# Kernel tuning notes

Hardware: AMD Instinct MI355X
Metric: run time of the kernel (lower is better)

## Reference

```python
import jax, jax.numpy as jnp
import numpy as np

SR = 44100
PRE_EMPH = 0.97
FRAME_LEN = int(0.02 * SR)      # 882
FRAME_HOP = FRAME_LEN // 2      # 441
N_FFT = 2048
EPS = 1e-10


def setup_inputs() -> dict:
    key = jax.random.key(0)
    k1, k2 = jax.random.split(key)
    waveform = jax.random.normal(k1, (16, 441000), dtype=jnp.float32)
    # librosa mel filterbank is a fixed nonnegative (n_mels, n_fft//2+1) matrix;
    # a random surrogate keeps the math (dense matmul) identical.
    mel_filters = jax.random.uniform(k2, (60, N_FFT // 2 + 1), dtype=jnp.float32)
    return {"waveform": waveform, "mel_filters": mel_filters}


def _mfdwc(waveform, mel_filters):
    dt = waveform.dtype
    # pre-emphasis: y[0]=x[0], y[t]=x[t]-0.97*x[t-1]
    emph = jnp.concatenate(
        [waveform[:, :1], waveform[:, 1:] - PRE_EMPH * waveform[:, :-1]], axis=1)
    L = emph.shape[1]
    n_frames = 1 + (L - FRAME_LEN) // FRAME_HOP  # static
    idx = jnp.arange(n_frames)[:, None] * FRAME_HOP + jnp.arange(FRAME_LEN)[None, :]
    frames = emph[:, idx]                                   # (B, T, 882)
    window = jnp.asarray(np.hamming(FRAME_LEN), dtype=dt)   # (882,)
    windowed = frames * window
    spec = jnp.fft.rfft(windowed, n=N_FFT, axis=-1)         # (B, T, 1025) complex
    power = jnp.real(spec) ** 2 + jnp.imag(spec) ** 2       # |FFT|^2
    mel = jnp.einsum('mf,btf->btm', mel_filters, power)     # (B, T, 60)
    logmel = jnp.log(mel + EPS)
    # 1-level Haar DWT along mel axis (pywt convention, even length):
    # cA = (x_even + x_odd)/sqrt(2), cD = (x_even - x_odd)/sqrt(2)
    sq2 = jnp.sqrt(jnp.asarray(2.0, dt))
    x_even, x_odd = logmel[..., 0::2], logmel[..., 1::2]
    cA = (x_even + x_odd) / sq2                             # (B, T, 30)
    cD = (x_even - x_odd) / sq2                             # (B, T, 30)
    # delta (window=3, edge-padded): d[t] = a[clamp(t+1)] - a[clamp(t-1)]
    fwd = jnp.concatenate([cA[:, 1:], cA[:, -1:]], axis=1)
    bwd = jnp.concatenate([cA[:, :1], cA[:, :-1]], axis=1)
    delta = fwd - bwd
    feats = jnp.concatenate([cA, delta, cD], axis=-1)       # (B, T, 90)
    mean = jnp.mean(feats, axis=1)
    std = jnp.std(feats, axis=1, ddof=1)                    # torch.std unbiased
    return jnp.concatenate([mean, std], axis=1)             # (B, 180)


def reference(waveform, mel_filters):
    return _mfdwc(waveform, mel_filters)
```

## Files before the change

### kernel.cpp

```cpp
#include <hip/hip_runtime.h>
#include <hip/hip_bf16.h>
#include <math.h>

#define FRAME_LEN 882
#define FRAME_HOP 441
#define NFFT 2048
#define NFRAMES 999
#define NBATCH 16
#define NMEL 60
#define WAVE_LEN 441000
#define PRE_EMPH 0.97f
#define EPS 1e-10f
#define NROWS (NBATCH * NFRAMES)
#define NPANEL 999
#define KPAD 1056
#define NKC 33
#define PANEL_ELEMS (NKC * 512)
#define PANEL_BYTES (PANEL_ELEMS * 2)
#define PI_F 3.14159265358979323846f

#define PADI(i) ((i) + ((i) >> 4))

__device__ __forceinline__ int frag_off(int m, int k) {
  return ((k >> 5) * 512) | (((k >> 3) & 3) * 128) | (m * 8) | (k & 7);
}

typedef float vf2 __attribute__((ext_vector_type(2)));
__device__ __forceinline__ vf2 mkv(float x, float y){ vf2 r; r.x = x; r.y = y; return r; }
__device__ __forceinline__ vf2 cmul(vf2 a, vf2 b){ return a.xx * b + mkv(-a.y, a.y) * b.yx; }
__device__ __forceinline__ vf2 rotni(vf2 z){ return mkv(z.y, -z.x); }

__device__ __forceinline__ void dif_group16(vf2* x, vf2 t1, bool zerohi) {
  const vf2 C81 = mkv(0.9238795325f, -0.3826834324f);
  const vf2 C82 = mkv(0.7071067812f, -0.7071067812f);
  const vf2 C83 = mkv(0.3826834324f, -0.9238795325f);
  vf2 w0 = t1, w1 = cmul(t1, C81), w2 = cmul(t1, C82), w3 = cmul(t1, C83);
  vf2 ws1[8] = {w0, w1, w2, w3, rotni(w0), rotni(w1), rotni(w2), rotni(w3)};
  if (zerohi) {
#pragma unroll
    for (int k = 0; k < 8; ++k) x[k + 8] = cmul(x[k], ws1[k]);
  } else {
#pragma unroll
    for (int k = 0; k < 8; ++k) {
      vf2 u = x[k], v = x[k + 8];
      x[k] = u + v;
      x[k + 8] = cmul(u - v, ws1[k]);
    }
  }
  vf2 t2 = cmul(t1, t1);
  vf2 v1 = cmul(t2, C82);
  vf2 ws2[4] = {t2, v1, rotni(t2), rotni(v1)};
#pragma unroll
  for (int h = 0; h < 2; ++h) {
#pragma unroll
    for (int k = 0; k < 4; ++k) {
      vf2 u = x[h*8 + k], v = x[h*8 + k + 4];
      x[h*8 + k] = u + v;
      x[h*8 + k + 4] = cmul(u - v, ws2[k]);
    }
  }
  vf2 t4 = cmul(t2, t2);
  vf2 t4r = rotni(t4);
#pragma unroll
  for (int h = 0; h < 4; ++h) {
    vf2 a = x[h*4 + 0], b = x[h*4 + 2];
    x[h*4 + 0] = a + b; x[h*4 + 2] = cmul(a - b, t4);
    a = x[h*4 + 1]; b = x[h*4 + 3];
    x[h*4 + 1] = a + b; x[h*4 + 3] = cmul(a - b, t4r);
  }
  vf2 t8 = cmul(t4, t4);
#pragma unroll
  for (int j = 0; j < 8; ++j) {
    vf2 a = x[2*j], b = x[2*j + 1];
    x[2*j] = a + b; x[2*j + 1] = cmul(a - b, t8);
  }
}

__device__ __forceinline__ void dif8(vf2* y) {
  const vf2 c1 = mkv(0.7071067812f, -0.7071067812f);
  const vf2 c3 = mkv(-0.7071067812f, -0.7071067812f);
  vf2 u, v;
  u=y[0]; v=y[4]; y[0]=u+v; y[4]=u-v;
  u=y[1]; v=y[5]; y[1]=u+v; y[5]=cmul(u-v, c1);
  u=y[2]; v=y[6]; y[2]=u+v; y[6]=rotni(u-v);
  u=y[3]; v=y[7]; y[3]=u+v; y[7]=cmul(u-v, c3);
  u=y[0]; v=y[2]; y[0]=u+v; y[2]=u-v;
  u=y[1]; v=y[3]; y[1]=u+v; y[3]=rotni(u-v);
  u=y[4]; v=y[6]; y[4]=u+v; y[6]=u-v;
  u=y[5]; v=y[7]; y[5]=u+v; y[7]=rotni(u-v);
  u=y[0]; v=y[1]; y[0]=u+v; y[1]=u-v;
  u=y[2]; v=y[3]; y[2]=u+v; y[3]=u-v;
  u=y[4]; v=y[5]; y[4]=u+v; y[5]=u-v;
  u=y[6]; v=y[7]; y[6]=u+v; y[7]=u-v;
}

__global__ __launch_bounds__(256) void fft_pow_kernel(
    const float* __restrict__ wav, const float* __restrict__ filt,
    __hip_bfloat16* __restrict__ powrF, __hip_bfloat16* __restrict__ filtbF)
{
  __shared__ vf2 lds2[2][NFFT + (NFFT >> 4)];
  const int id = blockIdx.x;

  if (id >= 4000) {
    const int mm = id - 4000;
    __hip_bfloat16* qp = filtbF + (size_t)(mm >> 4) * PANEL_ELEMS;
    const int m = mm & 15;
    for (int k = threadIdx.x; k < KPAD; k += 256) {
      float v = (mm < NMEL && k < 1025) ? filt[mm * 1025 + k] : 0.f;
      qp[frag_off(m, k)] = __float2bfloat16(v);
    }
    return;
  }

  const int t   = threadIdx.x;
  const int fid = t >> 7;
  const int tt  = t & 127;
  vf2* lds = lds2[fid];

  const int P  = id * 2 + fid;
  const int b  = P & 15;
  const int t0 = 2 * (P >> 4), t1f = t0 + 1;
  const bool has1 = (t1f < NFRAMES);
  const float* w = wav + (size_t)b * WAVE_LEN;
  const int s0 = t0 * FRAME_HOP;
  int s1 = t1f * FRAME_HOP;
  if (s1 > WAVE_LEN - FRAME_LEN) s1 = WAVE_LEN - FRAME_LEN;

  vf2 x[16];
  {
    float sB, cB, sD, cD;
    __sincosf(6.283185307179586f * (float)tt / 881.0f, &sB, &cB);
    __sincosf(6.283185307179586f * 128.0f / 881.0f, &sD, &cD);
    vf2 cur  = mkv(cB, sB);
    vf2 step = mkv(cD, sD);
#pragma unroll
    for (int k = 0; k < 7; ++k) {
      int i = k * 128 + tt;
      float v1 = 0.f, v2 = 0.f;
      if (i < FRAME_LEN) {
        float win = 0.54f - 0.46f * cur.x;
        int s = s0 + i;
        float e1 = (s > 0) ? (w[s] - PRE_EMPH * w[s - 1]) : w[s];
        v1 = e1 * win;
        int ss = s1 + i;
        v2 = (w[ss] - PRE_EMPH * w[ss - 1]) * win;
      }
      x[k] = mkv(v1, v2);
      cur = cmul(cur, step);
    }
#pragma unroll
    for (int k = 7; k < 16; ++k) x[k] = mkv(0.f, 0.f);
  }

  {
    float sA, cA;
    __sincosf(-PI_F * (float)tt / 1024.0f, &sA, &cA);
    dif_group16(x, mkv(cA, sA), true);
  }
#pragma unroll
  for (int k = 0; k < 16; ++k) lds[PADI(k * 128 + tt)] = x[k];
  __syncthreads();

  {
    const int Q = tt >> 3, r = tt & 7;
    const int base = Q * 128 + r;
#pragma unroll
    for (int k = 0; k < 16; ++k) x[k] = lds[PADI(base + k * 8)];
    float sA, cA;
    __sincosf(-PI_F * (float)r / 64.0f, &sA, &cA);
    dif_group16(x, mkv(cA, sA), false);
#pragma unroll
    for (int k = 0; k < 16; ++k) lds[PADI(base + k * 8)] = x[k];
  }
  __syncthreads();

  {
    vf2 ya[8], yb[8];
#pragma unroll
    for (int j = 0; j < 8; ++j) {
      ya[j] = lds[PADI(16 * tt + j)];
      yb[j] = lds[PADI(16 * tt + 8 + j)];
    }
    dif8(ya);
    dif8(yb);
    __syncthreads();
    const int r7 = (int)(__brev((unsigned)tt) >> 25);
    const int RA[8] = {0, 8, 4, 12, 2, 10, 6, 14};
    const int RB[8] = {1, 9, 5, 13, 3, 11, 7, 15};
#pragma unroll
    for (int j = 0; j < 8; ++j) {
      lds[PADI(RA[j] * 128 + r7)] = ya[j];
      lds[PADI(RB[j] * 128 + r7)] = yb[j];
    }
  }
  __syncthreads();

  const int r0g = b * NFRAMES + t0;
  const int r1g = r0g + 1;
  __hip_bfloat16* q0 = powrF + (size_t)(r0g >> 4) * PANEL_ELEMS;
  const int m0 = r0g & 15;
  __hip_bfloat16* q1 = powrF + (size_t)(r1g >> 4) * PANEL_ELEMS;
  const int m1 = r1g & 15;
#pragma unroll
  for (int c = 0; c < 8; ++c) {
    int f = c * 128 + tt;
    int mir = (NFFT - f) & (NFFT - 1);
    vf2 z = lds[PADI(f)];
    vf2 y = lds[PADI(mir)];
    float f1r = z.x + y.x, f1i = z.y - y.y;
    float f2r = z.y + y.y, f2i = y.x - z.x;
    float pw1 = 0.25f * (f1r * f1r + f1i * f1i);
    float pw2 = 0.25f * (f2r * f2r + f2i * f2i);
    q0[frag_off(m0, f)] = __float2bfloat16(pw1);
    if (has1) q1[frag_off(m1, f)] = __float2bfloat16(pw2);
  }
  if (tt == 0) {
    vf2 z = lds[PADI(1024)];
    q0[frag_off(m0, 1024)] = __float2bfloat16(z.x * z.x);
    if (has1) q1[frag_off(m1, 1024)] = __float2bfloat16(z.y * z.y);
  }
  if (tt < KPAD - 1025) {
    int f = 1025 + tt;
    q0[frag_off(m0, f)] = __float2bfloat16(0.f);
    if (has1) q1[frag_off(m1, f)] = __float2bfloat16(0.f);
  }
}

typedef __attribute__((ext_vector_type(8))) short short8x;
typedef __attribute__((ext_vector_type(4))) float float4x;

#define PPB 2

__global__ __launch_bounds__(256) void melgemm_kernel(
    const __hip_bfloat16* __restrict__ powrF,
    const __hip_bfloat16* __restrict__ filtbF,
    float* __restrict__ logmelT)
{
  __shared__ __hip_bfloat16 As[2][PANEL_ELEMS];
  const int tid  = threadIdx.x;
  const int wave = tid >> 6, lane = tid & 63;
  const int p0 = blockIdx.x * PPB;

  short8x Breg[NKC];
  {
    const __hip_bfloat16* pB = filtbF + (size_t)wave * PANEL_ELEMS + lane * 8;
#pragma unroll
    for (int kc = 0; kc < NKC; ++kc)
      Breg[kc] = *(const short8x*)(pB + kc * 512);
  }

  auto stage = [&](int buf, int p) {
    const unsigned char* src =
        (const unsigned char*)(powrF + (size_t)p * PANEL_ELEMS);
    unsigned char* dst = (unsigned char*)As[buf];
#pragma unroll
    for (int r = 0; r < 9; ++r) {
      const int off = r * 4096 + tid * 16;
      if (off < PANEL_BYTES) {
        __builtin_amdgcn_global_load_lds(
            (const __attribute__((address_space(1))) unsigned int*)(src + off),
            (__attribute__((address_space(3))) unsigned int*)(dst + off),
            16, 0, 0);
      }
    }
  };

  stage(0, p0);
  __syncthreads();

  const int mel  = wave * 16 + (lane & 15);
  const int rsub = (lane >> 4) * 4;

  for (int i = 0; i < PPB; ++i) {
    const int p = p0 + i;
    if (p >= NPANEL) break;
    const bool more = (i + 1 < PPB) && (p + 1 < NPANEL);
    if (more) stage((i + 1) & 1, p + 1);

    const __hip_bfloat16* A = As[i & 1];
    float4x acc0 = {0.f, 0.f, 0.f, 0.f};
    float4x acc1 = {0.f, 0.f, 0.f, 0.f};
#pragma unroll
    for (int kc = 0; kc < 16; ++kc) {
      short8x a0 = *(const short8x*)(&A[kc * 512 + lane * 8]);
      short8x a1 = *(const short8x*)(&A[(kc + 16) * 512 + lane * 8]);
      acc0 = __builtin_amdgcn_mfma_f32_16x16x32_bf16(a0, Breg[kc], acc0, 0, 0, 0);
      acc1 = __builtin_amdgcn_mfma_f32_16x16x32_bf16(a1, Breg[kc + 16], acc1, 0, 0, 0);
    }
    {
      short8x a = *(const short8x*)(&A[32 * 512 + lane * 8]);
      acc0 = __builtin_amdgcn_mfma_f32_16x16x32_bf16(a, Breg[32], acc0, 0, 0, 0);
    }

    if (mel < NMEL) {
#pragma unroll
      for (int reg = 0; reg < 4; ++reg) {
        int row = p * 16 + rsub + reg;
        float vv = acc0[reg] + acc1[reg];
        logmelT[(size_t)mel * NROWS + row] = __logf(vv + EPS);
      }
    }
    if (more) __syncthreads();
  }
}

__global__ __launch_bounds__(256) void stats_kernel(
    const float* __restrict__ lmT, float* __restrict__ out)
{
  __shared__ float red[4];
  const int j   = blockIdx.x;
  const int b   = blockIdx.y;
  const int tid = threadIdx.x;
  const int base = b * NFRAMES;
  const float inv_sq2 = 0.7071067811865475f;
  const bool v3 = (tid < NFRAMES - 768);

  float f0, f1, f2, f3;
  if (j < 30) {
    const float* e = lmT + (size_t)(2 * j) * NROWS + base;
    const float* o = lmT + (size_t)(2 * j + 1) * NROWS + base;
    f0 = (e[tid]       + o[tid])       * inv_sq2;
    f1 = (e[tid + 256] + o[tid + 256]) * inv_sq2;
    f2 = (e[tid + 512] + o[tid + 512]) * inv_sq2;
    f3 = v3 ? (e[tid + 768] + o[tid + 768]) * inv_sq2 : 0.f;
  } else if (j < 60) {
    const int m = j - 30;
    const float* e = lmT + (size_t)(2 * m) * NROWS + base;
    const float* o = lmT + (size_t)(2 * m + 1) * NROWS + base;
    auto dl = [&](int t) -> float {
      int tp = (t + 1 > NFRAMES - 1) ? (NFRAMES - 1) : (t + 1);
      int tm = (t - 1 < 0) ? 0 : (t - 1);
      return ((e[tp] + o[tp]) - (e[tm] + o[tm])) * inv_sq2;
    };
    f0 = dl(tid);
    f1 = dl(tid + 256);
    f2 = dl(tid + 512);
    f3 = v3 ? dl(tid + 768) : 0.f;
  } else {
    const int m = j - 60;
    const float* e = lmT + (size_t)(2 * m) * NROWS + base;
    const float* o = lmT + (size_t)(2 * m + 1) * NROWS + base;
    f0 = (e[tid]       - o[tid])       * inv_sq2;
    f1 = (e[tid + 256] - o[tid + 256]) * inv_sq2;
    f2 = (e[tid + 512] - o[tid + 512]) * inv_sq2;
    f3 = v3 ? (e[tid + 768] - o[tid + 768]) * inv_sq2 : 0.f;
  }

  float s = f0 + f1 + f2 + f3;
  for (int o2 = 32; o2 > 0; o2 >>= 1) s += __shfl_xor(s, o2, 64);
  if ((tid & 63) == 0) red[tid >> 6] = s;
  __syncthreads();
  float mean = (red[0] + red[1] + red[2] + red[3]) / (float)NFRAMES;
  __syncthreads();

  float d0 = f0 - mean, d1 = f1 - mean, d2 = f2 - mean;
  float d3 = v3 ? (f3 - mean) : 0.f;
  float s2 = d0 * d0 + d1 * d1 + d2 * d2 + d3 * d3;
  for (int o2 = 32; o2 > 0; o2 >>= 1) s2 += __shfl_xor(s2, o2, 64);
  if ((tid & 63) == 0) red[tid >> 6] = s2;
  __syncthreads();
  float var = (red[0] + red[1] + red[2] + red[3]) / (float)(NFRAMES - 1);

  if (tid == 0) {
    out[b * 180 + j]      = mean;
    out[b * 180 + 90 + j] = sqrtf(var);
  }
}

extern "C" void kernel_launch(void* const* d_in, const int* in_sizes, int n_in,
                              void* d_out, int out_size, void* d_ws, size_t ws_size,
                              hipStream_t stream) {
  const float* wav  = (const float*)d_in[0];
  const float* filt = (const float*)d_in[1];
  float* out = (float*)d_out;

  unsigned char* ws = (unsigned char*)d_ws;
  __hip_bfloat16* powrF  = (__hip_bfloat16*)(ws);
  size_t off = (size_t)NPANEL * PANEL_ELEMS * 2;
  __hip_bfloat16* filtbF = (__hip_bfloat16*)(ws + off);
  off += (size_t)4 * PANEL_ELEMS * 2;
  float* logmelT = (float*)(ws + off);

  fft_pow_kernel<<<4064, 256, 0, stream>>>(wav, filt, powrF, filtbF);
  melgemm_kernel<<<500, 256, 0, stream>>>(powrF, filtbF, logmelT);
  stats_kernel<<<dim3(90, NBATCH), 256, 0, stream>>>(logmelT, out);
}
```

Measured before the change: 112.9 us.

## Run each FFT pair on a single 64-thread wavefront with two columns per thread

The FFT kernel moves from 256-thread blocks that each handle two frame pairs with 128 threads apiece to 64-thread blocks that handle one frame pair, with each thread processing two columns (tt and tt+64) at every stage. Having one wavefront per FFT means its three __syncthreads barriers only synchronise a single wave, which lowers barrier cost, and more instruction-level parallelism is available per thread. The cost is roughly double the register pressure per thread, since x and y arrays of 16 complex values are both live, and the grid grows to 8064 small blocks, which may limit occupancy.

```diff
diff --git a/kernel.cpp b/kernel.cpp
--- a/kernel.cpp
+++ b/kernel.cpp
@@ -94,30 +94,28 @@
   u=y[6]; v=y[7]; y[6]=u+v; y[7]=u-v;
 }
 
-__global__ __launch_bounds__(256) void fft_pow_kernel(
+__global__ __launch_bounds__(64, 2) void fft_pow_kernel(
     const float* __restrict__ wav, const float* __restrict__ filt,
     __hip_bfloat16* __restrict__ powrF, __hip_bfloat16* __restrict__ filtbF)
 {
-  __shared__ vf2 lds2[2][NFFT + (NFFT >> 4)];
+  __shared__ vf2 lds[NFFT + (NFFT >> 4)];
   const int id = blockIdx.x;
 
-  if (id >= 4000) {
-    const int mm = id - 4000;
+  if (id >= 8000) {
+    const int mm = id - 8000;
     __hip_bfloat16* qp = filtbF + (size_t)(mm >> 4) * PANEL_ELEMS;
     const int m = mm & 15;
-    for (int k = threadIdx.x; k < KPAD; k += 256) {
+    for (int k = threadIdx.x; k < KPAD; k += 64) {
       float v = (mm < NMEL && k < 1025) ? filt[mm * 1025 + k] : 0.f;
       qp[frag_off(m, k)] = __float2bfloat16(v);
     }
     return;
   }
 
-  const int t   = threadIdx.x;
-  const int fid = t >> 7;
-  const int tt  = t & 127;
-  vf2* lds = lds2[fid];
-
-  const int P  = id * 2 + fid;
+  const int tt = threadIdx.x;
+  const int ub = tt + 64;
+
+  const int P  = id;
   const int b  = P & 15;
   const int t0 = 2 * (P >> 4), t1f = t0 + 1;
   const bool has1 = (t1f < NFRAMES);
@@ -126,71 +124,100 @@
   int s1 = t1f * FRAME_HOP;
   if (s1 > WAVE_LEN - FRAME_LEN) s1 = WAVE_LEN - FRAME_LEN;
 
-  vf2 x[16];
+  vf2 x[16], y[16];
   {
-    float sB, cB, sD, cD;
-    __sincosf(6.283185307179586f * (float)tt / 881.0f, &sB, &cB);
+    float sA, cA, sB, cB, sD, cD;
+    __sincosf(6.283185307179586f * (float)tt / 881.0f, &sA, &cA);
+    __sincosf(6.283185307179586f * (float)ub / 881.0f, &sB, &cB);
     __sincosf(6.283185307179586f * 128.0f / 881.0f, &sD, &cD);
-    vf2 cur  = mkv(cB, sB);
+    vf2 curA = mkv(cA, sA), curB = mkv(cB, sB);
     vf2 step = mkv(cD, sD);
 #pragma unroll
     for (int k = 0; k < 7; ++k) {
-      int i = k * 128 + tt;
-      float v1 = 0.f, v2 = 0.f;
-      if (i < FRAME_LEN) {
-        float win = 0.54f - 0.46f * cur.x;
+      {
+        int i = k * 128 + tt;
+        float win = 0.54f - 0.46f * curA.x;
         int s = s0 + i;
         float e1 = (s > 0) ? (w[s] - PRE_EMPH * w[s - 1]) : w[s];
-        v1 = e1 * win;
+        float v1 = e1 * win;
         int ss = s1 + i;
-        v2 = (w[ss] - PRE_EMPH * w[ss - 1]) * win;
+        float v2 = (w[ss] - PRE_EMPH * w[ss - 1]) * win;
+        x[k] = mkv(v1, v2);
+        curA = cmul(curA, step);
       }
-      x[k] = mkv(v1, v2);
-      cur = cmul(cur, step);
-    }
-#pragma unroll
-    for (int k = 7; k < 16; ++k) x[k] = mkv(0.f, 0.f);
+      {
+        int i = k * 128 + ub;
+        float v1 = 0.f, v2 = 0.f;
+        if (i < FRAME_LEN) {
+          float win = 0.54f - 0.46f * curB.x;
+          int s = s0 + i;
+          v1 = (w[s] - PRE_EMPH * w[s - 1]) * win;
+          int ss = s1 + i;
+          v2 = (w[ss] - PRE_EMPH * w[ss - 1]) * win;
+        }
+        y[k] = mkv(v1, v2);
+        curB = cmul(curB, step);
+      }
+    }
+#pragma unroll
+    for (int k = 7; k < 16; ++k) { x[k] = mkv(0.f, 0.f); y[k] = mkv(0.f, 0.f); }
   }
 
   {
-    float sA, cA;
-    __sincosf(-PI_F * (float)tt / 1024.0f, &sA, &cA);
-    dif_group16(x, mkv(cA, sA), true);
-  }
-#pragma unroll
-  for (int k = 0; k < 16; ++k) lds[PADI(k * 128 + tt)] = x[k];
+    float s_, c_;
+    __sincosf(-PI_F * (float)tt / 1024.0f, &s_, &c_);
+    dif_group16(x, mkv(c_, s_), true);
+    __sincosf(-PI_F * (float)ub / 1024.0f, &s_, &c_);
+    dif_group16(y, mkv(c_, s_), true);
+  }
+#pragma unroll
+  for (int k = 0; k < 16; ++k) {
+    lds[PADI(k * 128 + tt)] = x[k];
+    lds[PADI(k * 128 + ub)] = y[k];
+  }
   __syncthreads();
 
   {
     const int Q = tt >> 3, r = tt & 7;
-    const int base = Q * 128 + r;
-#pragma unroll
-    for (int k = 0; k < 16; ++k) x[k] = lds[PADI(base + k * 8)];
-    float sA, cA;
-    __sincosf(-PI_F * (float)r / 64.0f, &sA, &cA);
-    dif_group16(x, mkv(cA, sA), false);
-#pragma unroll
-    for (int k = 0; k < 16; ++k) lds[PADI(base + k * 8)] = x[k];
+    const int baseA = Q * 128 + r;
+    const int baseB = baseA + 1024;
+#pragma unroll
+    for (int k = 0; k < 16; ++k) x[k] = lds[PADI(baseA + k * 8)];
+#pragma unroll
+    for (int k = 0; k < 16; ++k) y[k] = lds[PADI(baseB + k * 8)];
+    float s_, c_;
+    __sincosf(-PI_F * (float)r / 64.0f, &s_, &c_);
+    vf2 t1 = mkv(c_, s_);
+    dif_group16(x, t1, false);
+    dif_group16(y, t1, false);
+#pragma unroll
+    for (int k = 0; k < 16; ++k) lds[PADI(baseA + k * 8)] = x[k];
+#pragma unroll
+    for (int k = 0; k < 16; ++k) lds[PADI(baseB + k * 8)] = y[k];
   }
   __syncthreads();
 
   {
-    vf2 ya[8], yb[8];
+    vf2 a0[8], a1[8], b0[8], b1[8];
 #pragma unroll
     for (int j = 0; j < 8; ++j) {
-      ya[j] = lds[PADI(16 * tt + j)];
-      yb[j] = lds[PADI(16 * tt + 8 + j)];
-    }
-    dif8(ya);
-    dif8(yb);
+      a0[j] = lds[PADI(16 * tt + j)];
+      a1[j] = lds[PADI(16 * tt + 8 + j)];
+      b0[j] = lds[PADI(16 * tt + 1024 + j)];
+      b1[j] = lds[PADI(16 * tt + 1024 + 8 + j)];
+    }
+    dif8(a0); dif8(a1); dif8(b0); dif8(b1);
     __syncthreads();
-    const int r7 = (int)(__brev((unsigned)tt) >> 25);
+    const int r7A = (int)(__brev((unsigned)tt) >> 25);
+    const int r7B = (int)(__brev((unsigned)ub) >> 25);
     const int RA[8] = {0, 8, 4, 12, 2, 10, 6, 14};
     const int RB[8] = {1, 9, 5, 13, 3, 11, 7, 15};
 #pragma unroll
     for (int j = 0; j < 8; ++j) {
-      lds[PADI(RA[j] * 128 + r7)] = ya[j];
-      lds[PADI(RB[j] * 128 + r7)] = yb[j];
+      lds[PADI(RA[j] * 128 + r7A)] = a0[j];
+      lds[PADI(RB[j] * 128 + r7A)] = a1[j];
+      lds[PADI(RA[j] * 128 + r7B)] = b0[j];
+      lds[PADI(RB[j] * 128 + r7B)] = b1[j];
     }
   }
   __syncthreads();
@@ -203,16 +230,30 @@
   const int m1 = r1g & 15;
 #pragma unroll
   for (int c = 0; c < 8; ++c) {
-    int f = c * 128 + tt;
-    int mir = (NFFT - f) & (NFFT - 1);
-    vf2 z = lds[PADI(f)];
-    vf2 y = lds[PADI(mir)];
-    float f1r = z.x + y.x, f1i = z.y - y.y;
-    float f2r = z.y + y.y, f2i = y.x - z.x;
-    float pw1 = 0.25f * (f1r * f1r + f1i * f1i);
-    float pw2 = 0.25f * (f2r * f2r + f2i * f2i);
-    q0[frag_off(m0, f)] = __float2bfloat16(pw1);
-    if (has1) q1[frag_off(m1, f)] = __float2bfloat16(pw2);
+    {
+      int f = c * 128 + tt;
+      int mir = (NFFT - f) & (NFFT - 1);
+      vf2 z = lds[PADI(f)];
+      vf2 yv = lds[PADI(mir)];
+      float f1r = z.x + yv.x, f1i = z.y - yv.y;
+      float f2r = z.y + yv.y, f2i = yv.x - z.x;
+      float pw1 = 0.25f * (f1r * f1r + f1i * f1i);
+      float pw2 = 0.25f * (f2r * f2r + f2i * f2i);
+      q0[frag_off(m0, f)] = __float2bfloat16(pw1);
+      if (has1) q1[frag_off(m1, f)] = __float2bfloat16(pw2);
+    }
+    {
+      int f = c * 128 + ub;
+      int mir = (NFFT - f) & (NFFT - 1);
+      vf2 z = lds[PADI(f)];
+      vf2 yv = lds[PADI(mir)];
+      float f1r = z.x + yv.x, f1i = z.y - yv.y;
+      float f2r = z.y + yv.y, f2i = yv.x - z.x;
+      float pw1 = 0.25f * (f1r * f1r + f1i * f1i);
+      float pw2 = 0.25f * (f2r * f2r + f2i * f2i);
+      q0[frag_off(m0, f)] = __float2bfloat16(pw1);
+      if (has1) q1[frag_off(m1, f)] = __float2bfloat16(pw2);
+    }
   }
   if (tt == 0) {
     vf2 z = lds[PADI(1024)];
@@ -381,7 +422,7 @@
   off += (size_t)4 * PANEL_ELEMS * 2;
   float* logmelT = (float*)(ws + off);
 
-  fft_pow_kernel<<<4064, 256, 0, stream>>>(wav, filt, powrF, filtbF);
+  fft_pow_kernel<<<8064, 64, 0, stream>>>(wav, filt, powrF, filtbF);
   melgemm_kernel<<<500, 256, 0, stream>>>(powrF, filtbF, logmelT);
   stats_kernel<<<dim3(90, NBATCH), 256, 0, stream>>>(logmelT, out);
 }
```

Result: slower. 128.0 us (+13.4%).
